# Kernel tuning notes

Hardware: AMD Instinct MI355X
Metric: run time of the kernel (lower is better)

Reference implementation:

```python
import jax, jax.numpy as jnp
import numpy as np

NX = 41                      # cube side: 2*r_max/voxel + 1 with r_max=6.0, voxel=0.3
VOXEL = 0.3
R_MAX = 6.0
MIN_DIST = 0.8
MIN_SEP = max(1, int(round(MIN_DIST / VOXEL)))   # 3 voxels
K = 4                        # topk_per_channel
NEG = -1.0e9                 # fp32 sentinel used by the torch module
VALID_THRESH = -1.0e8


def setup_inputs() -> dict:
    key = jax.random.key(0)
    B, N, C = 1, 128, 4
    G = NX ** 3
    ax = np.arange(NX)
    ii, jj, kk = np.meshgrid(ax, ax, ax, indexing='ij')
    coords = np.stack([ii, jj, kk], axis=-1).reshape(-1, 3)          # [G,3] integer voxel coords
    center = (NX - 1) / 2.0
    grid_xyz = ((coords - center) * VOXEL).astype(np.float32)        # [G,3] local Angstrom coords
    sphere_mask = np.linalg.norm(grid_xyz, axis=-1) <= R_MAX         # [G] bool
    k1, k2, k3 = jax.random.split(key, 3)
    density = jax.random.normal(k1, (B, N, C, G), jnp.float32)
    A = jax.random.normal(k2, (B, N, 3, 3), jnp.float32)
    Rmats, _ = jnp.linalg.qr(A)                                      # proper-ish rotation matrices
    tpos = jax.random.normal(k3, (B, N, 3), jnp.float32)
    node_mask = jnp.ones((B, N), jnp.float32)
    return dict(density=density,
                grid_xyz=jnp.asarray(grid_xyz),
                sphere_mask=jnp.asarray(sphere_mask),
                coords_int=jnp.asarray(coords, jnp.int32),
                Rmats=Rmats, tpos=tpos, node_mask=node_mask)


def extract_peaks(density, grid_xyz, sphere_mask, coords_int):
    # density: [B,N,C,G]; iterative argmax peak-picking with Chebyshev NMS suppression.
    v0 = jnp.where(sphere_mask[None, None, None, :], density, NEG)
    cx = coords_int[:, 0][None, None, None, :]   # [1,1,1,G]
    cy = coords_int[:, 1][None, None, None, :]
    cz = coords_int[:, 2][None, None, None, :]

    def step(v, _):
        idx = jnp.argmax(v, axis=-1)                                   # [B,N,C]
        score = jnp.take_along_axis(v, idx[..., None], axis=-1)[..., 0]
        valid = score > VALID_THRESH
        xyz = grid_xyz[idx]                                            # [B,N,C,3]
        ijk = coords_int[idx]                                          # [B,N,C,3]
        # Chebyshev (max-abs) voxel distance to the picked peak, per axis to avoid a [.,G,3] temp
        d = jnp.maximum(jnp.maximum(jnp.abs(cx - ijk[..., 0:1]),
                                    jnp.abs(cy - ijk[..., 1:2])),
                        jnp.abs(cz - ijk[..., 2:3]))                    # [B,N,C,G]
        suppress = (d <= MIN_SEP) & valid[..., None]
        v = jnp.where(suppress, NEG, v)
        out = (jnp.where(valid, score, NEG),
               jnp.where(valid[..., None], xyz, 0.0),
               valid)
        return v, out

    _, (scores, xyz, mask) = jax.lax.scan(step, v0, None, length=K)
    # K is leading scan axis -> move to axis 3 giving [B,N,C,K,...]
    return (jnp.moveaxis(xyz, 0, 3), jnp.moveaxis(scores, 0, 3), jnp.moveaxis(mask, 0, 3))


def reference(density, grid_xyz, sphere_mask, coords_int, Rmats, tpos, node_mask):
    peaks_xyz, peaks_score, peaks_mask = extract_peaks(density, grid_xyz, sphere_mask, coords_int)
    # local -> global frame: R @ x + t
    coords_global = jnp.einsum('bnij,bnckj->bncki', Rmats, peaks_xyz) + tpos[:, :, None, None, :]
    m = node_mask[..., None, None, None]                                # [B,N,1,1,1]
    coords_local = peaks_xyz * m
    coords_global = coords_global * m
    scores = peaks_score * node_mask[..., None, None]
    mask = peaks_mask & node_mask.astype(bool)[..., None, None]
    return coords_local, coords_global, scores, mask
```

## Files before the change

### kernel.cpp

```cpp
#include <hip/hip_runtime.h>

#define G_VOX  68921
#define GMAX   68920
#define NSEG   272
#define MWORDS 2176
#define NEGV (-1.0e9f)
#define VTH  (-1.0e8f)

__device__ __forceinline__ bool sphere_bit(const float* __restrict__ gxyz, int e) {
    if (e >= G_VOX) return false;
    float gx = gxyz[e * 3 + 0];
    float gy = gxyz[e * 3 + 1];
    float gz = gxyz[e * 3 + 2];
    float s  = __fadd_rn(__fadd_rn(__fmul_rn(gx, gx), __fmul_rn(gy, gy)),
                         __fmul_rn(gz, gz));
    return (__fsqrt_rn(s) <= 6.0f);
}

__global__ __launch_bounds__(256) void build_mask(
    const float* __restrict__ gxyz, unsigned int* __restrict__ mask)
{
    int idx = blockIdx.x * 256 + threadIdx.x;
    unsigned long long bal = __ballot(sphere_bit(gxyz, idx));
    int lane = threadIdx.x & 63;
    if (lane == 0)       mask[idx >> 5] = (unsigned int)bal;
    else if (lane == 32) mask[idx >> 5] = (unsigned int)(bal >> 32);
}

__device__ __forceinline__ void seg_scan8(
    const float* __restrict__ dens, const unsigned int* smask,
    int s, int h, int l8, int eclamp, float& bv, int& bi)
{
    const int ebase = h + 256 * s + 4 * l8;
    const int sh    = ebase & 31;
    const int wd0   = ebase >> 5;
    bv = NEGV; bi = ebase;

    float4       dq[8];
    unsigned int bq[8];
    unsigned int wprev = smask[wd0];
    #pragma unroll
    for (int q = 0; q < 8; ++q) {
        const int e = ebase + 32 * q;
        const unsigned int wnext = smask[wd0 + q + 1];
        unsigned long long mw = ((unsigned long long)wnext << 32) | wprev;
        bq[q] = (unsigned int)(mw >> sh) & 0xFu;
        wprev = wnext;
        const int ec = (e + 3 <= GMAX) ? e : eclamp;
        dq[q] = *reinterpret_cast<const float4*>(dens + ec);
    }
    #pragma unroll
    for (int q = 0; q < 8; ++q) {
        const int e = ebase + 32 * q;
        float v0 = (bq[q] & 1u) ? dq[q].x : NEGV;
        float v1 = (bq[q] & 2u) ? dq[q].y : NEGV;
        float v2 = (bq[q] & 4u) ? dq[q].z : NEGV;
        float v3 = (bq[q] & 8u) ? dq[q].w : NEGV;
        if (v0 > bv) { bv = v0; bi = e;     }
        if (v1 > bv) { bv = v1; bi = e + 1; }
        if (v2 > bv) { bv = v2; bi = e + 2; }
        if (v3 > bv) { bv = v3; bi = e + 3; }
    }
    #pragma unroll
    for (int off = 4; off > 0; off >>= 1) {
        float ov = __shfl_xor(bv, off);
        int   oi = __shfl_xor(bi, off);
        if (ov > bv || (ov == bv && oi < bi)) { bv = ov; bi = oi; }
    }
}

__global__ __launch_bounds__(512) void fused_peaks(
    const float* __restrict__ density,
    const float* __restrict__ gxyz,
    const unsigned int* __restrict__ maskg,
    const float* __restrict__ Rm, const float* __restrict__ tp,
    const float* __restrict__ nmask,
    float* __restrict__ out)
{
    __shared__ unsigned int smask[MWORDS + 2];
    __shared__ float sval[NSEG];
    __shared__ int   sidx[NSEG];
    __shared__ int   flag[NSEG];
    __shared__ int   list[104];
    __shared__ int   nlist;
    __shared__ float rv[8];
    __shared__ int   ri[8];
    __shared__ float pval[4];
    __shared__ int   pidx[4];
    __shared__ int   pki[4], pkj[4], pkk[4];

    const int tid  = threadIdx.x;
    const int nc   = blockIdx.x;
    const int n    = nc >> 2;
    const int h    = (-nc) & 3;
    const int lane = tid & 63;
    const int w    = tid >> 6;
    const int s8   = lane >> 3;
    const int l8   = lane & 7;
    const float* dens = density + (size_t)nc * G_VOX;
    const int eclamp = h + ((GMAX - 3 - h) & ~3);

    for (int i = tid; i < MWORDS + 2; i += 512) smask[i] = (i < MWORDS) ? maskg[i] : 0u;
    for (int i = tid; i < NSEG; i += 512) flag[i] = 0;
    __syncthreads();

    for (int g = w; g < 34; g += 8) {
        const int s = g * 8 + s8;
        float bv; int bi;
        seg_scan8(dens, smask, s, h, l8, eclamp, bv, bi);
        if (l8 == 0) { sval[s] = bv; sidx[s] = bi; }
    }
    __syncthreads();

    for (int p = 0; p < 4; ++p) {
        float bv = -INFINITY;
        int   bi = 0x7FFFFFFF;
        if (tid < NSEG) { bv = sval[tid]; bi = sidx[tid]; }
        #pragma unroll
        for (int off = 32; off > 0; off >>= 1) {
            float ov = __shfl_down(bv, off);
            int   oi = __shfl_down(bi, off);
            if (ov > bv || (ov == bv && oi < bi)) { bv = ov; bi = oi; }
        }
        if (lane == 0) { rv[w] = bv; ri[w] = bi; }
        __syncthreads();
        if (w == 0) {
            bv = (lane < 8) ? rv[lane] : -INFINITY;
            bi = (lane < 8) ? ri[lane] : 0x7FFFFFFF;
            #pragma unroll
            for (int off = 4; off > 0; off >>= 1) {
                float ov = __shfl_down(bv, off);
                int   oi = __shfl_down(bi, off);
                if (ov > bv || (ov == bv && oi < bi)) { bv = ov; bi = oi; }
            }
            if (lane == 0) {
                pval[p] = bv;
                pidx[p] = bi;
                int pi = bi / 1681;
                int rr = bi - pi * 1681;
                int pj = rr / 41;
                pki[p] = pi; pkj[p] = pj; pkk[p] = rr - pj * 41;
                nlist = 0;
            }
        }
        __syncthreads();

        if (p < 3 && pval[p] > VTH) {
            if (tid < 49) {
                int di = tid / 7 - 3, dj = tid % 7 - 3;
                int ii = pki[p] + di, jj = pkj[p] + dj;
                if (ii >= 0 && ii <= 40 && jj >= 0 && jj <= 40) {
                    int k0 = pkk[p] - 3; if (k0 < 0)  k0 = 0;
                    int k1 = pkk[p] + 3; if (k1 > 40) k1 = 40;
                    int b0  = ii * 1681 + jj * 41 + k0;
                    int cnt = k1 - k0 + 1;
                    unsigned long long m = ((1ull << cnt) - 1ull) << (b0 & 31);
                    int w0 = b0 >> 5;
                    atomicAnd(&smask[w0], ~(unsigned int)m);
                    unsigned int hi = (unsigned int)(m >> 32);
                    if (hi) atomicAnd(&smask[w0 + 1], ~hi);
                    int s0 = (b0 > h) ? (b0 - h) >> 8 : 0;
                    int s1 = (b0 + cnt - 1 > h) ? (b0 + cnt - 1 - h) >> 8 : 0;
                    if (atomicMax(&flag[s0], p + 1) < p + 1) {
                        int q = atomicAdd(&nlist, 1); list[q] = s0;
                    }
                    if (s1 != s0 && atomicMax(&flag[s1], p + 1) < p + 1) {
                        int q = atomicAdd(&nlist, 1); list[q] = s1;
                    }
                }
            }
            __syncthreads();
            const int cnt = nlist;
            for (int base = 0; base < cnt; base += 64) {
                const int slot = base + w * 8 + s8;
                if (slot < cnt) {
                    const int s = list[slot];
                    float bv2; int bi2;
                    seg_scan8(dens, smask, s, h, l8, eclamp, bv2, bi2);
                    if (l8 == 0) { sval[s] = bv2; sidx[s] = bi2; }
                }
            }
        }
        __syncthreads();
    }

    if (tid < 4) {
        const int k   = tid;
        const float val = pval[k];
        const int   idx = pidx[k];
        const bool valid = val > VTH;
        float gx = 0.0f, gy = 0.0f, gz = 0.0f;
        if (valid) {
            gx = gxyz[idx * 3 + 0];
            gy = gxyz[idx * 3 + 1];
            gz = gxyz[idx * 3 + 2];
        }
        const float nm = nmask[n];
        const float* R = Rm + n * 9;
        const float* t = tp + n * 3;
        float wx = R[0] * gx + R[1] * gy + R[2] * gz + t[0];
        float wy = R[3] * gx + R[4] * gy + R[5] * gz + t[1];
        float wz = R[6] * gx + R[7] * gy + R[8] * gz + t[2];

        const size_t o3 = ((size_t)nc * 4 + k) * 3;
        out[o3 + 0] = gx * nm;
        out[o3 + 1] = gy * nm;
        out[o3 + 2] = gz * nm;
        out[6144 + o3 + 0] = wx * nm;
        out[6144 + o3 + 1] = wy * nm;
        out[6144 + o3 + 2] = wz * nm;
        const size_t o1 = (size_t)nc * 4 + k;
        out[12288 + o1] = (valid ? val : NEGV) * nm;
        out[14336 + o1] = (valid && nm != 0.0f) ? 1.0f : 0.0f;
    }
}

extern "C" void kernel_launch(void* const* d_in, const int* in_sizes, int n_in,
                              void* d_out, int out_size, void* d_ws, size_t ws_size,
                              hipStream_t stream) {
    const float* density  = (const float*)d_in[0];
    const float* grid_xyz = (const float*)d_in[1];
    const float* Rm    = (const float*)d_in[4];
    const float* tpos  = (const float*)d_in[5];
    const float* nmask = (const float*)d_in[6];
    float* out = (float*)d_out;

    unsigned int* mask = (unsigned int*)d_ws;

    build_mask<<<dim3(272), dim3(256), 0, stream>>>(grid_xyz, mask);
    fused_peaks<<<dim3(512), dim3(512), 0, stream>>>(density, grid_xyz, mask,
                                                     Rm, tpos, nmask, out);
}
```

Baseline: 226.6 us.

## Split initial segment scan into separate high-parallelism kernel writing max table

The initial per-segment argmax scan over each (node,channel) density volume moves out of the 512-block NMS kernel into a new 2048-block kernel. Each block handles a quarter of the segments and writes segment maxima and indices to a workspace table. The NMS kernel then loads this table instead of scanning. The aim is to fill more CUs during the bandwidth-bound scan, at the cost of an extra launch and a small table round-trip through global memory. It falls back to the fused kernel when the workspace is too small.

Result: slower. 231.7 us (+2.3%).

```diff
diff --git a/kernel.cpp b/kernel.cpp
--- a/kernel.cpp
+++ b/kernel.cpp
@@ -3,9 +3,13 @@
 #define G_VOX  68921
 #define GMAX   68920
 #define NSEG   272
+#define SEG_PER_PART 68
 #define MWORDS 2176
 #define NEGV (-1.0e9f)
 #define VTH  (-1.0e8f)
+
+#define WS_TAB_OFF 16384
+#define WS_NEEDED  (WS_TAB_OFF + 512 * NSEG * 4 * 2)
 
 __device__ __forceinline__ bool sphere_bit(const float* __restrict__ gxyz, int e) {
     if (e >= G_VOX) return false;
@@ -27,22 +31,18 @@
     else if (lane == 32) mask[idx >> 5] = (unsigned int)(bal >> 32);
 }
 
-__device__ __forceinline__ void seg_scan8(
-    const float* __restrict__ dens, const unsigned int* smask,
-    int s, int h, int l8, int eclamp, float& bv, int& bi)
+__device__ __forceinline__ void seg_scan8_core(
+    const float* __restrict__ dens, const unsigned int* smw,
+    int ebase, int sh, int eclamp, float& bv, int& bi)
 {
-    const int ebase = h + 256 * s + 4 * l8;
-    const int sh    = ebase & 31;
-    const int wd0   = ebase >> 5;
     bv = NEGV; bi = ebase;
-
     float4       dq[8];
     unsigned int bq[8];
-    unsigned int wprev = smask[wd0];
+    unsigned int wprev = smw[0];
     #pragma unroll
     for (int q = 0; q < 8; ++q) {
         const int e = ebase + 32 * q;
-        const unsigned int wnext = smask[wd0 + q + 1];
+        const unsigned int wnext = smw[q + 1];
         unsigned long long mw = ((unsigned long long)wnext << 32) | wprev;
         bq[q] = (unsigned int)(mw >> sh) & 0xFu;
         wprev = wnext;
@@ -69,10 +69,51 @@
     }
 }
 
-__global__ __launch_bounds__(512) void fused_peaks(
+__global__ __launch_bounds__(256) void scan_table(
+    const float* __restrict__ density,
+    const unsigned int* __restrict__ maskg,
+    float* __restrict__ wval, int* __restrict__ widx)
+{
+    __shared__ unsigned int lm[SEG_PER_PART * 8 + 2];
+    const int bid  = blockIdx.x;
+    const int nc   = bid >> 2;
+    const int part = bid & 3;
+    const int s0   = part * SEG_PER_PART;
+    const int h    = (-nc) & 3;
+    const int tid  = threadIdx.x;
+    const int lane = tid & 63;
+    const int w    = tid >> 6;
+    const int s8   = lane >> 3;
+    const int l8   = lane & 7;
+    const float* dens = density + (size_t)nc * G_VOX;
+    const int eclamp = h + ((GMAX - 3 - h) & ~3);
+    const int wbase  = 8 * s0;
+
+    for (int i = tid; i < SEG_PER_PART * 8 + 2; i += 256) {
+        const int gw = wbase + i;
+        lm[i] = (gw < MWORDS) ? maskg[gw] : 0u;
+    }
+    __syncthreads();
+
+    const int sh = h + 4 * l8;
+    #pragma unroll
+    for (int j = 0; j < 3; ++j) {
+        const int sl = j * 32 + w * 8 + s8;
+        if (sl < SEG_PER_PART) {
+            const int s = s0 + sl;
+            const int ebase = h + 256 * s + 4 * l8;
+            float bv; int bi;
+            seg_scan8_core(dens, lm + 8 * sl, ebase, sh, eclamp, bv, bi);
+            if (l8 == 0) { wval[nc * NSEG + s] = bv; widx[nc * NSEG + s] = bi; }
+        }
+    }
+}
+
+__global__ __launch_bounds__(512) void nms_peaks(
     const float* __restrict__ density,
     const float* __restrict__ gxyz,
     const unsigned int* __restrict__ maskg,
+    const float* __restrict__ wval, const int* __restrict__ widx,
     const float* __restrict__ Rm, const float* __restrict__ tp,
     const float* __restrict__ nmask,
     float* __restrict__ out)
@@ -101,14 +142,10 @@
     const int eclamp = h + ((GMAX - 3 - h) & ~3);
 
     for (int i = tid; i < MWORDS + 2; i += 512) smask[i] = (i < MWORDS) ? maskg[i] : 0u;
-    for (int i = tid; i < NSEG; i += 512) flag[i] = 0;
-    __syncthreads();
-
-    for (int g = w; g < 34; g += 8) {
-        const int s = g * 8 + s8;
-        float bv; int bi;
-        seg_scan8(dens, smask, s, h, l8, eclamp, bv, bi);
-        if (l8 == 0) { sval[s] = bv; sidx[s] = bi; }
+    for (int i = tid; i < NSEG; i += 512) {
+        flag[i] = 0;
+        sval[i] = wval[nc * NSEG + i];
+        sidx[i] = widx[nc * NSEG + i];
     }
     __syncthreads();
 
@@ -175,8 +212,9 @@
                 const int slot = base + w * 8 + s8;
                 if (slot < cnt) {
                     const int s = list[slot];
+                    const int ebase = h + 256 * s + 4 * l8;
                     float bv2; int bi2;
-                    seg_scan8(dens, smask, s, h, l8, eclamp, bv2, bi2);
+                    seg_scan8_core(dens, smask + 8 * s, ebase, h + 4 * l8, eclamp, bv2, bi2);
                     if (l8 == 0) { sval[s] = bv2; sidx[s] = bi2; }
                 }
             }
@@ -215,6 +253,154 @@
     }
 }
 
+__global__ __launch_bounds__(512) void fused_peaks(
+    const float* __restrict__ density,
+    const float* __restrict__ gxyz,
+    const unsigned int* __restrict__ maskg,
+    const float* __restrict__ Rm, const float* __restrict__ tp,
+    const float* __restrict__ nmask,
+    float* __restrict__ out)
+{
+    __shared__ unsigned int smask[MWORDS + 2];
+    __shared__ float sval[NSEG];
+    __shared__ int   sidx[NSEG];
+    __shared__ int   flag[NSEG];
+    __shared__ int   list[104];
+    __shared__ int   nlist;
+    __shared__ float rv[8];
+    __shared__ int   ri[8];
+    __shared__ float pval[4];
+    __shared__ int   pidx[4];
+    __shared__ int   pki[4], pkj[4], pkk[4];
+
+    const int tid  = threadIdx.x;
+    const int nc   = blockIdx.x;
+    const int n    = nc >> 2;
+    const int h    = (-nc) & 3;
+    const int lane = tid & 63;
+    const int w    = tid >> 6;
+    const int s8   = lane >> 3;
+    const int l8   = lane & 7;
+    const float* dens = density + (size_t)nc * G_VOX;
+    const int eclamp = h + ((GMAX - 3 - h) & ~3);
+
+    for (int i = tid; i < MWORDS + 2; i += 512) smask[i] = (i < MWORDS) ? maskg[i] : 0u;
+    for (int i = tid; i < NSEG; i += 512) flag[i] = 0;
+    __syncthreads();
+
+    for (int g = w; g < 34; g += 8) {
+        const int s = g * 8 + s8;
+        const int ebase = h + 256 * s + 4 * l8;
+        float bv; int bi;
+        seg_scan8_core(dens, smask + 8 * s, ebase, h + 4 * l8, eclamp, bv, bi);
+        if (l8 == 0) { sval[s] = bv; sidx[s] = bi; }
+    }
+    __syncthreads();
+
+    for (int p = 0; p < 4; ++p) {
+        float bv = -INFINITY;
+        int   bi = 0x7FFFFFFF;
+        if (tid < NSEG) { bv = sval[tid]; bi = sidx[tid]; }
+        #pragma unroll
+        for (int off = 32; off > 0; off >>= 1) {
+            float ov = __shfl_down(bv, off);
+            int   oi = __shfl_down(bi, off);
+            if (ov > bv || (ov == bv && oi < bi)) { bv = ov; bi = oi; }
+        }
+        if (lane == 0) { rv[w] = bv; ri[w] = bi; }
+        __syncthreads();
+        if (w == 0) {
+            bv = (lane < 8) ? rv[lane] : -INFINITY;
+            bi = (lane < 8) ? ri[lane] : 0x7FFFFFFF;
+            #pragma unroll
+            for (int off = 4; off > 0; off >>= 1) {
+                float ov = __shfl_down(bv, off);
+                int   oi = __shfl_down(bi, off);
+                if (ov > bv || (ov == bv && oi < bi)) { bv = ov; bi = oi; }
+            }
+            if (lane == 0) {
+                pval[p] = bv;
+                pidx[p] = bi;
+                int pi = bi / 1681;
+                int rr = bi - pi * 1681;
+                int pj = rr / 41;
+                pki[p] = pi; pkj[p] = pj; pkk[p] = rr - pj * 41;
+                nlist = 0;
+            }
+        }
+        __syncthreads();
+
+        if (p < 3 && pval[p] > VTH) {
+            if (tid < 49) {
+                int di = tid / 7 - 3, dj = tid % 7 - 3;
+                int ii = pki[p] + di, jj = pkj[p] + dj;
+                if (ii >= 0 && ii <= 40 && jj >= 0 && jj <= 40) {
+                    int k0 = pkk[p] - 3; if (k0 < 0)  k0 = 0;
+                    int k1 = pkk[p] + 3; if (k1 > 40) k1 = 40;
+                    int b0  = ii * 1681 + jj * 41 + k0;
+                    int cnt = k1 - k0 + 1;
+                    unsigned long long m = ((1ull << cnt) - 1ull) << (b0 & 31);
+                    int w0 = b0 >> 5;
+                    atomicAnd(&smask[w0], ~(unsigned int)m);
+                    unsigned int hi = (unsigned int)(m >> 32);
+                    if (hi) atomicAnd(&smask[w0 + 1], ~hi);
+                    int s0 = (b0 > h) ? (b0 - h) >> 8 : 0;
+                    int s1 = (b0 + cnt - 1 > h) ? (b0 + cnt - 1 - h) >> 8 : 0;
+                    if (atomicMax(&flag[s0], p + 1) < p + 1) {
+                        int q = atomicAdd(&nlist, 1); list[q] = s0;
+                    }
+                    if (s1 != s0 && atomicMax(&flag[s1], p + 1) < p + 1) {
+                        int q = atomicAdd(&nlist, 1); list[q] = s1;
+                    }
+                }
+            }
+            __syncthreads();
+            const int cnt = nlist;
+            for (int base = 0; base < cnt; base += 64) {
+                const int slot = base + w * 8 + s8;
+                if (slot < cnt) {
+                    const int s = list[slot];
+                    const int ebase = h + 256 * s + 4 * l8;
+                    float bv2; int bi2;
+                    seg_scan8_core(dens, smask + 8 * s, ebase, h + 4 * l8, eclamp, bv2, bi2);
+                    if (l8 == 0) { sval[s] = bv2; sidx[s] = bi2; }
+                }
+            }
+        }
+        __syncthreads();
+    }
+
+    if (tid < 4) {
+        const int k   = tid;
+        const float val = pval[k];
+        const int   idx = pidx[k];
+        const bool valid = val > VTH;
+        float gx = 0.0f, gy = 0.0f, gz = 0.0f;
+        if (valid) {
+            gx = gxyz[idx * 3 + 0];
+            gy = gxyz[idx * 3 + 1];
+            gz = gxyz[idx * 3 + 2];
+        }
+        const float nm = nmask[n];
+        const float* R = Rm + n * 9;
+        const float* t = tp + n * 3;
+        float wx = R[0] * gx + R[1] * gy + R[2] * gz + t[0];
+        float wy = R[3] * gx + R[4] * gy + R[5] * gz + t[1];
+        float wz = R[6] * gx + R[7] * gy + R[8] * gz + t[2];
+
+        const size_t o3 = ((size_t)nc * 4 + k) * 3;
+        out[o3 + 0] = gx * nm;
+        out[o3 + 1] = gy * nm;
+        out[o3 + 2] = gz * nm;
+        out[6144 + o3 + 0] = wx * nm;
+        out[6144 + o3 + 1] = wy * nm;
+        out[6144 + o3 + 2] = wz * nm;
+        const size_t o1 = (size_t)nc * 4 + k;
+        out[12288 + o1] = (valid ? val : NEGV) * nm;
+        out[14336 + o1] = (valid && nm != 0.0f) ? 1.0f : 0.0f;
+    }
+}
+
 extern "C" void kernel_launch(void* const* d_in, const int* in_sizes, int n_in,
                               void* d_out, int out_size, void* d_ws, size_t ws_size,
                               hipStream_t stream) {
@@ -228,6 +414,15 @@
     unsigned int* mask = (unsigned int*)d_ws;
 
     build_mask<<<dim3(272), dim3(256), 0, stream>>>(grid_xyz, mask);
-    fused_peaks<<<dim3(512), dim3(512), 0, stream>>>(density, grid_xyz, mask,
-                                                     Rm, tpos, nmask, out);
-}
+
+    if (ws_size >= (size_t)WS_NEEDED) {
+        float* wval = (float*)((char*)d_ws + WS_TAB_OFF);
+        int*   widx = (int*)((char*)d_ws + WS_TAB_OFF + 512 * NSEG * 4);
+        scan_table<<<dim3(2048), dim3(256), 0, stream>>>(density, mask, wval, widx);
+        nms_peaks<<<dim3(512), dim3(512), 0, stream>>>(density, grid_xyz, mask,
+                                                       wval, widx, Rm, tpos, nmask, out);
+    } else {
+        fused_peaks<<<dim3(512), dim3(512), 0, stream>>>(density, grid_xyz, mask,
+                                                         Rm, tpos, nmask, out);
+    }
+}
```
